# Kernel tuning notes

Measured on AMD Instinct MI355X. Metric: run time of the kernel, lower is better.

## Reference

```python
import jax, jax.numpy as jnp
import numpy as np

NUM_TOKENS = 65536
D_MODEL = 2048
NUM_EXPERTS = 64


def setup_inputs() -> dict:
    key = jax.random.key(0)
    kx, kw = jax.random.split(key)
    x = jax.random.normal(kx, (NUM_TOKENS, D_MODEL), dtype=jnp.float32)
    W = jax.random.normal(kw, (NUM_EXPERTS, D_MODEL), dtype=jnp.float32) * (1.0 / np.sqrt(D_MODEL))
    return {"x": x, "W": W}


def reference(x, W):
    # logits = x @ W^T : [T, E]
    logits = jnp.einsum("td,ed->te", x, W)
    probs = jax.nn.softmax(logits, axis=-1)
    top_idx = jnp.argmax(probs, axis=-1)                     # [T]
    expert_indices = jax.nn.one_hot(top_idx, NUM_EXPERTS, dtype=jnp.int32)  # [T, E]
    top_prob = jnp.max(probs, axis=-1, keepdims=True)        # [T, 1]
    return expert_indices, top_prob, logits
```

## Files before the change

kernel.cpp:

```cpp
#include <hip/hip_runtime.h>


constexpr int T_TOK = 65536;
constexpr int DM    = 2048;
constexpr int NE    = 64;
constexpr int BM    = 128;
constexpr int BK    = 64;
constexpr int NCH   = DM / BK;
constexpr int WPAD  = 72;
constexpr int PLANE = NE * WPAD;
constexpr int WBUF  = 3 * PLANE;

typedef __attribute__((ext_vector_type(8))) short bf16x8;
typedef __attribute__((ext_vector_type(4))) float f32x4;

__device__ __forceinline__ void split3(const f32x4& a, const f32x4& b,
                                       bf16x8& h, bf16x8& m, bf16x8& l) {
#pragma unroll
    for (int j = 0; j < 8; ++j) {
        const float xv = (j < 4) ? a[j] : b[j - 4];
        const unsigned u0 = __float_as_uint(xv);
        h[j] = (short)(u0 >> 16);
        const float r1 = xv - __uint_as_float(u0 & 0xFFFF0000u);
        const unsigned u1 = __float_as_uint(r1);
        m[j] = (short)(u1 >> 16);
        const float r2 = r1 - __uint_as_float(u1 & 0xFFFF0000u);
        l[j] = (short)(__float_as_uint(r2) >> 16);
    }
}

__global__ __launch_bounds__(256, 2)
void router_mfma(const float* __restrict__ x, const float* __restrict__ W,
                 float* __restrict__ onehot, float* __restrict__ topp,
                 float* __restrict__ logits)
{
    __shared__ __align__(16) unsigned short wlds[2 * WBUF];

    const int tid  = threadIdx.x;
    const int lane = tid & 63;
    const int wave = tid >> 6;
    const int r16  = lane & 15;
    const int quad = lane >> 4;

    const long blk_t0 = (long)blockIdx.x * BM;
    const long trow0  = blk_t0 + wave * 32 + r16;
    const long trow1  = trow0 + 16;

    const float* xp0 = x + trow0 * DM + quad * 8;
    const float* xp1 = x + trow1 * DM + quad * 8;

    const int we  = tid >> 2;
    const int wk0 = (tid & 3) * 16;
    const float* wp = W + (long)we * DM + wk0;
    const int wo = we * WPAD + wk0;

    f32x4 acc[2][4];
#pragma unroll
    for (int mt = 0; mt < 2; ++mt)
#pragma unroll
        for (int nt = 0; nt < 4; ++nt) acc[mt][nt] = (f32x4){0.f, 0.f, 0.f, 0.f};

    f32x4 xn[2][2][2];
    f32x4 wn[4];
    bf16x8 af[2][2][3];

#pragma unroll
    for (int mt = 0; mt < 2; ++mt)
#pragma unroll
        for (int ks = 0; ks < 2; ++ks) {
            const float* p = (mt ? xp1 : xp0) + ks * 32;
            xn[mt][ks][0] = *(const f32x4*)p;
            xn[mt][ks][1] = *(const f32x4*)(p + 4);
        }
#pragma unroll
    for (int j = 0; j < 4; ++j) wn[j] = *(const f32x4*)(wp + j * 4);

#pragma unroll
    for (int mt = 0; mt < 2; ++mt)
#pragma unroll
        for (int ks = 0; ks < 2; ++ks)
            split3(xn[mt][ks][0], xn[mt][ks][1],
                   af[mt][ks][0], af[mt][ks][1], af[mt][ks][2]);
    {
        bf16x8 h0, m0, l0, h1, m1, l1;
        split3(wn[0], wn[1], h0, m0, l0);
        split3(wn[2], wn[3], h1, m1, l1);
        unsigned short* wb = wlds;
        *(bf16x8*)(wb + 0 * PLANE + wo)     = h0;
        *(bf16x8*)(wb + 0 * PLANE + wo + 8) = h1;
        *(bf16x8*)(wb + 1 * PLANE + wo)     = m0;
        *(bf16x8*)(wb + 1 * PLANE + wo + 8) = m1;
        *(bf16x8*)(wb + 2 * PLANE + wo)     = l0;
        *(bf16x8*)(wb + 2 * PLANE + wo + 8) = l1;
    }
    __syncthreads();

    for (int kc = 0; kc < NCH; ++kc) {
        const int nxt = kc + 1;
        if (nxt < NCH) {
#pragma unroll
            for (int mt = 0; mt < 2; ++mt)
#pragma unroll
                for (int ks = 0; ks < 2; ++ks) {
                    const float* p = (mt ? xp1 : xp0) + nxt * BK + ks * 32;
                    xn[mt][ks][0] = *(const f32x4*)p;
                    xn[mt][ks][1] = *(const f32x4*)(p + 4);
                }
#pragma unroll
            for (int j = 0; j < 4; ++j) wn[j] = *(const f32x4*)(wp + nxt * BK + j * 4);
        }

        const unsigned short* wb = wlds + (kc & 1) * WBUF;
        const int bo = r16 * WPAD + quad * 8;
#pragma unroll
        for (int ks = 0; ks < 2; ++ks) {
#pragma unroll
            for (int nt = 0; nt < 4; ++nt) {
                const int eo = (nt * 16) * WPAD + bo + ks * 32;
                const bf16x8 bh = *(const bf16x8*)(wb + 0 * PLANE + eo);
                const bf16x8 bm = *(const bf16x8*)(wb + 1 * PLANE + eo);
                const bf16x8 bl = *(const bf16x8*)(wb + 2 * PLANE + eo);
#pragma unroll
                for (int mt = 0; mt < 2; ++mt) {
                    f32x4 c = acc[mt][nt];
                    c = __builtin_amdgcn_mfma_f32_16x16x32_bf16(af[mt][ks][0], bh, c, 0, 0, 0);
                    c = __builtin_amdgcn_mfma_f32_16x16x32_bf16(af[mt][ks][1], bh, c, 0, 0, 0);
                    c = __builtin_amdgcn_mfma_f32_16x16x32_bf16(af[mt][ks][2], bh, c, 0, 0, 0);
                    c = __builtin_amdgcn_mfma_f32_16x16x32_bf16(af[mt][ks][0], bm, c, 0, 0, 0);
                    c = __builtin_amdgcn_mfma_f32_16x16x32_bf16(af[mt][ks][1], bm, c, 0, 0, 0);
                    c = __builtin_amdgcn_mfma_f32_16x16x32_bf16(af[mt][ks][0], bl, c, 0, 0, 0);
                    acc[mt][nt] = c;
                }
            }
        }

        if (nxt < NCH) {
#pragma unroll
            for (int mt = 0; mt < 2; ++mt)
#pragma unroll
                for (int ks = 0; ks < 2; ++ks)
                    split3(xn[mt][ks][0], xn[mt][ks][1],
                           af[mt][ks][0], af[mt][ks][1], af[mt][ks][2]);
            bf16x8 h0, m0, l0, h1, m1, l1;
            split3(wn[0], wn[1], h0, m0, l0);
            split3(wn[2], wn[3], h1, m1, l1);
            unsigned short* wb2 = wlds + (nxt & 1) * WBUF;
            *(bf16x8*)(wb2 + 0 * PLANE + wo)     = h0;
            *(bf16x8*)(wb2 + 0 * PLANE + wo + 8) = h1;
            *(bf16x8*)(wb2 + 1 * PLANE + wo)     = m0;
            *(bf16x8*)(wb2 + 1 * PLANE + wo + 8) = m1;
            *(bf16x8*)(wb2 + 2 * PLANE + wo)     = l0;
            *(bf16x8*)(wb2 + 2 * PLANE + wo + 8) = l1;
        }
        __syncthreads();
    }

#pragma unroll
    for (int mt = 0; mt < 2; ++mt) {
#pragma unroll
        for (int reg = 0; reg < 4; ++reg) {
            const long t = blk_t0 + wave * 32 + mt * 16 + quad * 4 + reg;

            float mval = acc[mt][0][reg];
            int   mi   = r16;
#pragma unroll
            for (int nt = 1; nt < 4; ++nt) {
                const float v = acc[mt][nt][reg];
                if (v > mval) { mval = v; mi = nt * 16 + r16; }
            }
#pragma unroll
            for (int d = 1; d < 16; d <<= 1) {
                const float om = __shfl_xor(mval, d, 64);
                const int   oi = __shfl_xor(mi, d, 64);
                if (om > mval || (om == mval && oi < mi)) { mval = om; mi = oi; }
            }
            float s = 0.f;
#pragma unroll
            for (int nt = 0; nt < 4; ++nt) s += __expf(acc[mt][nt][reg] - mval);
#pragma unroll
            for (int d = 1; d < 16; d <<= 1) s += __shfl_xor(s, d, 64);

            const long ob = t * NE + r16;
#pragma unroll
            for (int nt = 0; nt < 4; ++nt) {
                logits[ob + nt * 16] = acc[mt][nt][reg];
                onehot[ob + nt * 16] = (nt * 16 + r16 == mi) ? 1.0f : 0.0f;
            }
            if (r16 == 0) topp[t] = 1.0f / s;
        }
    }
}

extern "C" void kernel_launch(void* const* d_in, const int* in_sizes, int n_in,
                              void* d_out, int out_size, void* d_ws, size_t ws_size,
                              hipStream_t stream)
{
    const float* x = (const float*)d_in[0];
    const float* W = (const float*)d_in[1];
    float* out = (float*)d_out;

    float* onehot = out;
    float* topp   = out + (long)T_TOK * NE;
    float* logits = topp + T_TOK;

    router_mfma<<<dim3(T_TOK / BM), dim3(256), 0, stream>>>(x, W, onehot, topp, logits);
}
```

Baseline: 730.4 us.

## Precompute W bf16x3 split in a prepass kernel with swizzled LDS layout

Adds a small prepass kernel that splits W into hi/mid/lo bf16 planes once and stores them pre-chunked and XOR-swizzled in the workspace. The main kernel then copies these planes straight into LDS instead of every block re-splitting W each K-chunk, and reads them through a swizzle rather than padding. It also packs the split with byte-permute instructions. The cost is an extra kernel launch and more global traffic for W (three bf16 planes instead of one fp32 copy), which stays small and cache-resident.

```diff
diff --git a/kernel.cpp b/kernel.cpp
--- a/kernel.cpp
+++ b/kernel.cpp
@@ -7,34 +7,65 @@
 constexpr int BM    = 128;
 constexpr int BK    = 64;
 constexpr int NCH   = DM / BK;
-constexpr int WPAD  = 72;
-constexpr int PLANE = NE * WPAD;
-constexpr int WBUF  = 3 * PLANE;
+constexpr int PLB   = NE * BK * 2;
+constexpr int CHB   = 3 * PLB;
 
 typedef __attribute__((ext_vector_type(8))) short bf16x8;
 typedef __attribute__((ext_vector_type(4))) float f32x4;
-
-__device__ __forceinline__ void split3(const f32x4& a, const f32x4& b,
-                                       bf16x8& h, bf16x8& m, bf16x8& l) {
-#pragma unroll
-    for (int j = 0; j < 8; ++j) {
-        const float xv = (j < 4) ? a[j] : b[j - 4];
-        const unsigned u0 = __float_as_uint(xv);
-        h[j] = (short)(u0 >> 16);
-        const float r1 = xv - __uint_as_float(u0 & 0xFFFF0000u);
-        const unsigned u1 = __float_as_uint(r1);
-        m[j] = (short)(u1 >> 16);
-        const float r2 = r1 - __uint_as_float(u1 & 0xFFFF0000u);
-        l[j] = (short)(__float_as_uint(r2) >> 16);
+typedef __attribute__((ext_vector_type(4))) unsigned int u32x4;
+
+__device__ __forceinline__ unsigned int pack_hi16(unsigned int lo, unsigned int hi) {
+    return __builtin_amdgcn_perm(hi, lo, 0x07060302u);
+}
+
+__device__ __forceinline__ void split3x8(const f32x4& a, const f32x4& b,
+                                         u32x4& h, u32x4& m, u32x4& l) {
+#pragma unroll
+    for (int p = 0; p < 4; ++p) {
+        const float x0 = (p < 2) ? a[2 * p]     : b[2 * p - 4];
+        const float x1 = (p < 2) ? a[2 * p + 1] : b[2 * p - 3];
+        const unsigned u00 = __float_as_uint(x0);
+        const unsigned u01 = __float_as_uint(x1);
+        h[p] = pack_hi16(u00, u01);
+        const float r10 = x0 - __uint_as_float(u00 & 0xFFFF0000u);
+        const float r11 = x1 - __uint_as_float(u01 & 0xFFFF0000u);
+        const unsigned u10 = __float_as_uint(r10);
+        const unsigned u11 = __float_as_uint(r11);
+        m[p] = pack_hi16(u10, u11);
+        const float r20 = r10 - __uint_as_float(u10 & 0xFFFF0000u);
+        const float r21 = r11 - __uint_as_float(u11 & 0xFFFF0000u);
+        l[p] = pack_hi16(__float_as_uint(r20), __float_as_uint(r21));
     }
 }
 
+__global__ __launch_bounds__(256)
+void wsplit(const float* __restrict__ W, unsigned char* __restrict__ wq)
+{
+    const int gid = blockIdx.x * 256 + threadIdx.x;
+    const int e   = gid >> 8;
+    const int g   = gid & 255;
+    const int k0  = g << 3;
+    const int kc  = k0 >> 6;
+    const int gi  = (k0 >> 3) & 7;
+
+    const float* p = W + (long)e * DM + k0;
+    const f32x4 a  = *(const f32x4*)p;
+    const f32x4 bb = *(const f32x4*)(p + 4);
+    u32x4 h, m, l;
+    split3x8(a, bb, h, m, l);
+
+    unsigned char* dst = wq + (long)kc * CHB + e * 128 + ((gi ^ (e & 7)) << 4);
+    *(u32x4*)(dst)           = h;
+    *(u32x4*)(dst + PLB)     = m;
+    *(u32x4*)(dst + 2 * PLB) = l;
+}
+
 __global__ __launch_bounds__(256, 2)
-void router_mfma(const float* __restrict__ x, const float* __restrict__ W,
+void router_mfma(const float* __restrict__ x, const unsigned char* __restrict__ wq,
                  float* __restrict__ onehot, float* __restrict__ topp,
                  float* __restrict__ logits)
 {
-    __shared__ __align__(16) unsigned short wlds[2 * WBUF];
+    __shared__ __align__(16) unsigned char wlds[2 * CHB];
 
     const int tid  = threadIdx.x;
     const int lane = tid & 63;
@@ -49,10 +80,7 @@
     const float* xp0 = x + trow0 * DM + quad * 8;
     const float* xp1 = x + trow1 * DM + quad * 8;
 
-    const int we  = tid >> 2;
-    const int wk0 = (tid & 3) * 16;
-    const float* wp = W + (long)we * DM + wk0;
-    const int wo = we * WPAD + wk0;
+    const unsigned char* wsrc = wq + tid * 16;
 
     f32x4 acc[2][4];
 #pragma unroll
@@ -61,8 +89,8 @@
         for (int nt = 0; nt < 4; ++nt) acc[mt][nt] = (f32x4){0.f, 0.f, 0.f, 0.f};
 
     f32x4 xn[2][2][2];
-    f32x4 wn[4];
-    bf16x8 af[2][2][3];
+    u32x4 af[2][2][3];
+    u32x4 wreg[6];
 
 #pragma unroll
     for (int mt = 0; mt < 2; ++mt)
@@ -73,27 +101,21 @@
             xn[mt][ks][1] = *(const f32x4*)(p + 4);
         }
 #pragma unroll
-    for (int j = 0; j < 4; ++j) wn[j] = *(const f32x4*)(wp + j * 4);
+    for (int it = 0; it < 6; ++it)
+        wreg[it] = *(const u32x4*)(wsrc + it * 4096);
 
 #pragma unroll
     for (int mt = 0; mt < 2; ++mt)
 #pragma unroll
         for (int ks = 0; ks < 2; ++ks)
-            split3(xn[mt][ks][0], xn[mt][ks][1],
-                   af[mt][ks][0], af[mt][ks][1], af[mt][ks][2]);
-    {
-        bf16x8 h0, m0, l0, h1, m1, l1;
-        split3(wn[0], wn[1], h0, m0, l0);
-        split3(wn[2], wn[3], h1, m1, l1);
-        unsigned short* wb = wlds;
-        *(bf16x8*)(wb + 0 * PLANE + wo)     = h0;
-        *(bf16x8*)(wb + 0 * PLANE + wo + 8) = h1;
-        *(bf16x8*)(wb + 1 * PLANE + wo)     = m0;
-        *(bf16x8*)(wb + 1 * PLANE + wo + 8) = m1;
-        *(bf16x8*)(wb + 2 * PLANE + wo)     = l0;
-        *(bf16x8*)(wb + 2 * PLANE + wo + 8) = l1;
-    }
+            split3x8(xn[mt][ks][0], xn[mt][ks][1],
+                     af[mt][ks][0], af[mt][ks][1], af[mt][ks][2]);
+#pragma unroll
+    for (int it = 0; it < 6; ++it)
+        *(u32x4*)(&wlds[tid * 16 + it * 4096]) = wreg[it];
     __syncthreads();
+
+    const int swz_r = (r16 & 7);
 
     for (int kc = 0; kc < NCH; ++kc) {
         const int nxt = kc + 1;
@@ -106,29 +128,34 @@
                     xn[mt][ks][0] = *(const f32x4*)p;
                     xn[mt][ks][1] = *(const f32x4*)(p + 4);
                 }
-#pragma unroll
-            for (int j = 0; j < 4; ++j) wn[j] = *(const f32x4*)(wp + nxt * BK + j * 4);
-        }
-
-        const unsigned short* wb = wlds + (kc & 1) * WBUF;
-        const int bo = r16 * WPAD + quad * 8;
+            const unsigned char* ws2 = wsrc + (long)nxt * CHB;
+#pragma unroll
+            for (int it = 0; it < 6; ++it)
+                wreg[it] = *(const u32x4*)(ws2 + it * 4096);
+        }
+
+        const unsigned char* wb = &wlds[(kc & 1) * CHB];
 #pragma unroll
         for (int ks = 0; ks < 2; ++ks) {
 #pragma unroll
             for (int nt = 0; nt < 4; ++nt) {
-                const int eo = (nt * 16) * WPAD + bo + ks * 32;
-                const bf16x8 bh = *(const bf16x8*)(wb + 0 * PLANE + eo);
-                const bf16x8 bm = *(const bf16x8*)(wb + 1 * PLANE + eo);
-                const bf16x8 bl = *(const bf16x8*)(wb + 2 * PLANE + eo);
+                const int eo = (nt * 16 + r16) * 128 +
+                               (((((ks << 2) | quad)) ^ swz_r) << 4);
+                const bf16x8 bh = *(const bf16x8*)(wb + eo);
+                const bf16x8 bm = *(const bf16x8*)(wb + PLB + eo);
+                const bf16x8 bl = *(const bf16x8*)(wb + 2 * PLB + eo);
 #pragma unroll
                 for (int mt = 0; mt < 2; ++mt) {
+                    const bf16x8 ah = __builtin_bit_cast(bf16x8, af[mt][ks][0]);
+                    const bf16x8 am = __builtin_bit_cast(bf16x8, af[mt][ks][1]);
+                    const bf16x8 al = __builtin_bit_cast(bf16x8, af[mt][ks][2]);
                     f32x4 c = acc[mt][nt];
-                    c = __builtin_amdgcn_mfma_f32_16x16x32_bf16(af[mt][ks][0], bh, c, 0, 0, 0);
-                    c = __builtin_amdgcn_mfma_f32_16x16x32_bf16(af[mt][ks][1], bh, c, 0, 0, 0);
-                    c = __builtin_amdgcn_mfma_f32_16x16x32_bf16(af[mt][ks][2], bh, c, 0, 0, 0);
-                    c = __builtin_amdgcn_mfma_f32_16x16x32_bf16(af[mt][ks][0], bm, c, 0, 0, 0);
-                    c = __builtin_amdgcn_mfma_f32_16x16x32_bf16(af[mt][ks][1], bm, c, 0, 0, 0);
-                    c = __builtin_amdgcn_mfma_f32_16x16x32_bf16(af[mt][ks][0], bl, c, 0, 0, 0);
+                    c = __builtin_amdgcn_mfma_f32_16x16x32_bf16(ah, bh, c, 0, 0, 0);
+                    c = __builtin_amdgcn_mfma_f32_16x16x32_bf16(am, bh, c, 0, 0, 0);
+                    c = __builtin_amdgcn_mfma_f32_16x16x32_bf16(al, bh, c, 0, 0, 0);
+                    c = __builtin_amdgcn_mfma_f32_16x16x32_bf16(ah, bm, c, 0, 0, 0);
+                    c = __builtin_amdgcn_mfma_f32_16x16x32_bf16(am, bm, c, 0, 0, 0);
+                    c = __builtin_amdgcn_mfma_f32_16x16x32_bf16(ah, bl, c, 0, 0, 0);
                     acc[mt][nt] = c;
                 }
             }
@@ -139,18 +166,12 @@
             for (int mt = 0; mt < 2; ++mt)
 #pragma unroll
                 for (int ks = 0; ks < 2; ++ks)
-                    split3(xn[mt][ks][0], xn[mt][ks][1],
-                           af[mt][ks][0], af[mt][ks][1], af[mt][ks][2]);
-            bf16x8 h0, m0, l0, h1, m1, l1;
-            split3(wn[0], wn[1], h0, m0, l0);
-            split3(wn[2], wn[3], h1, m1, l1);
-            unsigned short* wb2 = wlds + (nxt & 1) * WBUF;
-            *(bf16x8*)(wb2 + 0 * PLANE + wo)     = h0;
-            *(bf16x8*)(wb2 + 0 * PLANE + wo + 8) = h1;
-            *(bf16x8*)(wb2 + 1 * PLANE + wo)     = m0;
-            *(bf16x8*)(wb2 + 1 * PLANE + wo + 8) = m1;
-            *(bf16x8*)(wb2 + 2 * PLANE + wo)     = l0;
-            *(bf16x8*)(wb2 + 2 * PLANE + wo + 8) = l1;
+                    split3x8(xn[mt][ks][0], xn[mt][ks][1],
+                             af[mt][ks][0], af[mt][ks][1], af[mt][ks][2]);
+            unsigned char* wd = &wlds[(nxt & 1) * CHB + tid * 16];
+#pragma unroll
+            for (int it = 0; it < 6; ++it)
+                *(u32x4*)(wd + it * 4096) = wreg[it];
         }
         __syncthreads();
     }
@@ -195,6 +216,7 @@
                               void* d_out, int out_size, void* d_ws, size_t ws_size,
                               hipStream_t stream)
 {
+    (void)in_sizes; (void)n_in; (void)out_size; (void)ws_size;
     const float* x = (const float*)d_in[0];
     const float* W = (const float*)d_in[1];
     float* out = (float*)d_out;
@@ -203,5 +225,8 @@
     float* topp   = out + (long)T_TOK * NE;
     float* logits = topp + T_TOK;
 
-    router_mfma<<<dim3(T_TOK / BM), dim3(256), 0, stream>>>(x, W, onehot, topp, logits);
-}
+    unsigned char* wq = (unsigned char*)d_ws;
+
+    wsplit<<<dim3(64), dim3(256), 0, stream>>>(W, wq);
+    router_mfma<<<dim3(T_TOK / BM), dim3(256), 0, stream>>>(x, wq, onehot, topp, logits);
+}
```

Measured after the change: 721.5 us. Within noise of the previous version (-1.2%).
